# Performance work log

Hardware: AMD Instinct MI355X
Metric: run time of the kernel (lower is better)

Reference implementation:

```python
import jax, jax.numpy as jnp
import numpy as np

LATENT_DIM = 128
KQ_DIM = 32
B, N, K = 4, 16384, 64


def setup_inputs() -> dict:
    key = jax.random.key(0)
    k1, k2, k3, k4, k5, k6, k7 = jax.random.split(key, 7)
    return {
        "indices": jax.random.randint(k1, (3, B, N, K), 0, N, dtype=jnp.int64)
        if jax.config.jax_enable_x64 else jax.random.randint(k1, (3, B, N, K), 0, N, dtype=jnp.int32),
        "img": jax.random.normal(k2, (B, 3, 128, 128), dtype=jnp.float32),
        "features": jax.random.normal(k3, (B, N, LATENT_DIM), dtype=jnp.float32),
        "Wk": jax.random.normal(k4, (KQ_DIM, LATENT_DIM), dtype=jnp.float32) * 0.05,
        "bk": jax.random.normal(k5, (KQ_DIM,), dtype=jnp.float32) * 0.05,
        "Wq": jax.random.normal(k6, (KQ_DIM, LATENT_DIM), dtype=jnp.float32) * 0.05,
        "bq": jax.random.normal(k7, (KQ_DIM,), dtype=jnp.float32) * 0.05,
    }


def reference(indices, img, features, Wk, bk, Wq, bq):
    # features: [B, N, latent] -> keys/queries: [B, N, D]
    ks = jnp.einsum("bnl,dl->bnd", features, Wk) + bk
    qs = jnp.einsum("bnl,dl->bnd", features, Wq) + bq
    D = ks.shape[-1]
    # indices row 1 indexes keys, row 2 indexes queries (values in [0, N))
    x_idx = indices[1].reshape(B, N * K)  # [B, N*K]
    y_idx = indices[2].reshape(B, N * K)
    # gather along node axis: [B, N*K, D]
    x_feat = jnp.take_along_axis(ks, x_idx[:, :, None], axis=1)
    y_feat = jnp.take_along_axis(qs, y_idx[:, :, None], axis=1)
    # scaled dot product per edge -> [B, N, K]
    logits = (x_feat * y_feat).sum(axis=-1).reshape(B, N, K) * (D ** -0.5)
    return logits
```

## Files before the change

kernel.cpp:

```cpp
#include <hip/hip_runtime.h>
#include <hip/hip_fp16.h>

#define LATENT 128
#define DQK    32
#define BB     4
#define NN     16384
#define KK     64
#define TOTAL_EDGES (BB * NN * KK)
#define TOTAL_NODES (BB * NN)
#define PADF   132
#define EPT    4

__device__ __forceinline__ int dot4i8(int a, int b, int c) {
#if __has_builtin(__builtin_amdgcn_sdot4)
    return __builtin_amdgcn_sdot4(a, b, c, false);
#else
    c += ((a << 24) >> 24) * ((b << 24) >> 24);
    c += ((a << 16) >> 24) * ((b << 16) >> 24);
    c += ((a <<  8) >> 24) * ((b <<  8) >> 24);
    c += (a >> 24) * (b >> 24);
    return c;
#endif
}

__global__ __launch_bounds__(256, 2) void proj_kernel(
    const float* __restrict__ features,
    const float* __restrict__ Wk,
    const float* __restrict__ bk,
    const float* __restrict__ Wq,
    const float* __restrict__ bq,
    signed char* __restrict__ ks8,
    signed char* __restrict__ qs8,
    __half* __restrict__ sk,
    __half* __restrict__ sq)
{
    __shared__ float sf[64 * PADF];
    __shared__ float sw[64 * PADF];
    __shared__ float sb[64];

    const int t = threadIdx.x;
    const int node0 = blockIdx.x * 64;

    #pragma unroll
    for (int j = 0; j < 8; ++j) {
        int idx = t + j * 256;
        int r = idx >> 5;
        int c = idx & 31;
        const float4* src = (r < 32) ? (const float4*)Wk : (const float4*)Wq;
        float4 v = src[(size_t)(r & 31) * 32 + c];
        *(float4*)&sw[r * PADF + c * 4] = v;
    }
    if (t < 64) sb[t] = (t < 32) ? bk[t] : bq[t - 32];

    #pragma unroll
    for (int j = 0; j < 8; ++j) {
        int idx = t + j * 256;
        int r = idx >> 5;
        int c = idx & 31;
        float4 v = ((const float4*)(features + (size_t)(node0 + r) * LATENT))[c];
        *(float4*)&sf[r * PADF + c * 4] = v;
    }
    __syncthreads();

    const int tx = t & 15;
    const int ty = t >> 4;

    float acc[4][4];
    #pragma unroll
    for (int i = 0; i < 4; ++i)
        #pragma unroll
        for (int u = 0; u < 4; ++u) acc[i][u] = 0.f;

    #pragma unroll 4
    for (int kk = 0; kk < 32; ++kk) {
        float4 a[4], b[4];
        #pragma unroll
        for (int i = 0; i < 4; ++i)
            a[i] = *(const float4*)&sf[(ty * 4 + i) * PADF + kk * 4];
        #pragma unroll
        for (int u = 0; u < 4; ++u)
            b[u] = *(const float4*)&sw[(tx + 16 * u) * PADF + kk * 4];
        #pragma unroll
        for (int i = 0; i < 4; ++i)
            #pragma unroll
            for (int u = 0; u < 4; ++u)
                acc[i][u] += a[i].x * b[u].x + a[i].y * b[u].y
                           + a[i].z * b[u].z + a[i].w * b[u].w;
    }

    float vk0[4], vk1[4], vq0[4], vq1[4], mk[4], mq[4];
    #pragma unroll
    for (int i = 0; i < 4; ++i) {
        vk0[i] = acc[i][0] + sb[tx];
        vk1[i] = acc[i][1] + sb[tx + 16];
        vq0[i] = acc[i][2] + sb[tx + 32];
        vq1[i] = acc[i][3] + sb[tx + 48];
        mk[i] = fmaxf(fabsf(vk0[i]), fabsf(vk1[i]));
        mq[i] = fmaxf(fabsf(vq0[i]), fabsf(vq1[i]));
    }
    #pragma unroll
    for (int mask = 1; mask < 16; mask <<= 1) {
        #pragma unroll
        for (int i = 0; i < 4; ++i) {
            mk[i] = fmaxf(mk[i], __shfl_xor(mk[i], mask));
            mq[i] = fmaxf(mq[i], __shfl_xor(mq[i], mask));
        }
    }
    #pragma unroll
    for (int i = 0; i < 4; ++i) {
        const int node = node0 + ty * 4 + i;
        const float invk = (mk[i] > 0.f) ? 127.f / mk[i] : 0.f;
        const float invq = (mq[i] > 0.f) ? 127.f / mq[i] : 0.f;
        signed char* kr = ks8 + (size_t)node * 32;
        signed char* qr = qs8 + (size_t)node * 32;
        kr[tx]      = (signed char)__float2int_rn(vk0[i] * invk);
        kr[tx + 16] = (signed char)__float2int_rn(vk1[i] * invk);
        qr[tx]      = (signed char)__float2int_rn(vq0[i] * invq);
        qr[tx + 16] = (signed char)__float2int_rn(vq1[i] * invq);
        if (tx == 0) {
            sk[node] = __float2half(mk[i] * (1.f / 127.f));
            sq[node] = __float2half(mq[i] * (1.f / 127.f));
        }
    }
}

__global__ __launch_bounds__(512, 2) void edge_kernel(
    const int* __restrict__ xidx,
    const int* __restrict__ yidx,
    const signed char* __restrict__ ks8,
    const signed char* __restrict__ qs8,
    const __half* __restrict__ sk,
    const __half* __restrict__ sq,
    float* __restrict__ out)
{
    __shared__ __half ssk[NN];
    __shared__ __half ssq[NN];

    const int t = threadIdx.x;
    const int b = blockIdx.x >> 9;

    const uint4* gk = (const uint4*)(sk + (size_t)b * NN);
    const uint4* gq = (const uint4*)(sq + (size_t)b * NN);
    uint4* lk = (uint4*)ssk;
    uint4* lq = (uint4*)ssq;
    #pragma unroll
    for (int j = 0; j < 4; ++j) {
        lk[t + j * 512] = gk[t + j * 512];
        lq[t + j * 512] = gq[t + j * 512];
    }
    __syncthreads();

    const int base_e = (blockIdx.x & 511) * (512 * EPT);
    const int gbase  = b << 20;
    const size_t nodebase = (size_t)b << 14;

    int xs[EPT], ys[EPT];
    #pragma unroll
    for (int m = 0; m < EPT; ++m) {
        const int e = base_e + m * 512 + t;
        xs[m] = xidx[gbase + e];
        ys[m] = yidx[gbase + e];
    }
    __builtin_amdgcn_sched_barrier(0);

    uint4 kv0[EPT], kv1[EPT], qv0[EPT], qv1[EPT];
    const uint4* k4 = (const uint4*)ks8;
    const uint4* q4 = (const uint4*)qs8;
    #pragma unroll
    for (int m = 0; m < EPT; ++m) {
        const size_t xo = (nodebase + (size_t)xs[m]) << 1;
        const size_t yo = (nodebase + (size_t)ys[m]) << 1;
        kv0[m] = k4[xo];
        kv1[m] = k4[xo + 1];
        qv0[m] = q4[yo];
        qv1[m] = q4[yo + 1];
    }
    __builtin_amdgcn_sched_barrier(0);

    #pragma unroll
    for (int m = 0; m < EPT; ++m) {
        int d = 0;
        d = dot4i8((int)kv0[m].x, (int)qv0[m].x, d);
        d = dot4i8((int)kv0[m].y, (int)qv0[m].y, d);
        d = dot4i8((int)kv0[m].z, (int)qv0[m].z, d);
        d = dot4i8((int)kv0[m].w, (int)qv0[m].w, d);
        d = dot4i8((int)kv1[m].x, (int)qv1[m].x, d);
        d = dot4i8((int)kv1[m].y, (int)qv1[m].y, d);
        d = dot4i8((int)kv1[m].z, (int)qv1[m].z, d);
        d = dot4i8((int)kv1[m].w, (int)qv1[m].w, d);
        const float skx = __half2float(ssk[xs[m]]);
        const float sqy = __half2float(ssq[ys[m]]);
        const int e = base_e + m * 512 + t;
        out[gbase + e] = (float)d * skx * sqy * 0.17677669529663687f;
    }
}

extern "C" void kernel_launch(void* const* d_in, const int* in_sizes, int n_in,
                              void* d_out, int out_size, void* d_ws, size_t ws_size,
                              hipStream_t stream) {
    const int*   indices  = (const int*)d_in[0];
    const float* features = (const float*)d_in[2];
    const float* Wk       = (const float*)d_in[3];
    const float* bk       = (const float*)d_in[4];
    const float* Wq       = (const float*)d_in[5];
    const float* bq       = (const float*)d_in[6];
    float* out = (float*)d_out;

    signed char* ks8 = (signed char*)d_ws;
    signed char* qs8 = ks8 + (size_t)TOTAL_NODES * 32;
    __half* sk = (__half*)(qs8 + (size_t)TOTAL_NODES * 32);
    __half* sq = sk + TOTAL_NODES;

    const int* xidx = indices + (size_t)1 * TOTAL_EDGES;
    const int* yidx = indices + (size_t)2 * TOTAL_EDGES;

    proj_kernel<<<TOTAL_NODES / 64, 256, 0, stream>>>(
        features, Wk, bk, Wq, bq, ks8, qs8, sk, sq);
    edge_kernel<<<BB * 512, 512, 0, stream>>>(xidx, yidx, ks8, qs8, sk, sq, out);
}
```

Before: 74.24 us.

## Pipeline projection and edge stages per batch in a fused staged kernel

```diff
diff --git a/kernel.cpp b/kernel.cpp
--- a/kernel.cpp
+++ b/kernel.cpp
@@ -10,6 +10,8 @@
 #define TOTAL_NODES (BB * NN)
 #define PADF   132
 #define EPT    4
+#define PROJ_BLOCKS 256
+#define EDGE_BLOCKS 512
 
 __device__ __forceinline__ int dot4i8(int a, int b, int c) {
 #if __has_builtin(__builtin_amdgcn_sdot4)
@@ -23,175 +25,173 @@
 #endif
 }
 
-__global__ __launch_bounds__(256, 2) void proj_kernel(
+__global__ __launch_bounds__(512, 2) void stage_kernel(
     const float* __restrict__ features,
     const float* __restrict__ Wk,
     const float* __restrict__ bk,
     const float* __restrict__ Wq,
     const float* __restrict__ bq,
+    const int* __restrict__ xidx,
+    const int* __restrict__ yidx,
     signed char* __restrict__ ks8,
     signed char* __restrict__ qs8,
     __half* __restrict__ sk,
-    __half* __restrict__ sq)
+    __half* __restrict__ sq,
+    float* __restrict__ out,
+    int eb, int pb, int nProj)
 {
-    __shared__ float sf[64 * PADF];
-    __shared__ float sw[64 * PADF];
-    __shared__ float sb[64];
+    __shared__ __align__(16) unsigned char smem[67840];
 
     const int t = threadIdx.x;
-    const int node0 = blockIdx.x * 64;
-
-    #pragma unroll
-    for (int j = 0; j < 8; ++j) {
-        int idx = t + j * 256;
-        int r = idx >> 5;
-        int c = idx & 31;
-        const float4* src = (r < 32) ? (const float4*)Wk : (const float4*)Wq;
-        float4 v = src[(size_t)(r & 31) * 32 + c];
-        *(float4*)&sw[r * PADF + c * 4] = v;
-    }
-    if (t < 64) sb[t] = (t < 32) ? bk[t] : bq[t - 32];
-
-    #pragma unroll
-    for (int j = 0; j < 8; ++j) {
-        int idx = t + j * 256;
-        int r = idx >> 5;
-        int c = idx & 31;
-        float4 v = ((const float4*)(features + (size_t)(node0 + r) * LATENT))[c];
-        *(float4*)&sf[r * PADF + c * 4] = v;
-    }
-    __syncthreads();
-
-    const int tx = t & 15;
-    const int ty = t >> 4;
-
-    float acc[4][4];
-    #pragma unroll
-    for (int i = 0; i < 4; ++i)
-        #pragma unroll
-        for (int u = 0; u < 4; ++u) acc[i][u] = 0.f;
-
-    #pragma unroll 4
-    for (int kk = 0; kk < 32; ++kk) {
-        float4 a[4], b[4];
-        #pragma unroll
-        for (int i = 0; i < 4; ++i)
-            a[i] = *(const float4*)&sf[(ty * 4 + i) * PADF + kk * 4];
-        #pragma unroll
-        for (int u = 0; u < 4; ++u)
-            b[u] = *(const float4*)&sw[(tx + 16 * u) * PADF + kk * 4];
-        #pragma unroll
-        for (int i = 0; i < 4; ++i)
+
+    if ((int)blockIdx.x < nProj) {
+        float* sf = (float*)smem;
+        float* sw = sf + 64 * PADF;
+        float* sb = sw + 64 * PADF;
+
+        const int node0 = (pb << 14) + blockIdx.x * 64;
+
+        #pragma unroll
+        for (int j = 0; j < 4; ++j) {
+            int idx = t + j * 512;
+            int r = idx >> 5;
+            int c = idx & 31;
+            const float4* src = (r < 32) ? (const float4*)Wk : (const float4*)Wq;
+            float4 v = src[(size_t)(r & 31) * 32 + c];
+            *(float4*)&sw[r * PADF + c * 4] = v;
+        }
+        if (t < 64) sb[t] = (t < 32) ? bk[t] : bq[t - 32];
+
+        #pragma unroll
+        for (int j = 0; j < 4; ++j) {
+            int idx = t + j * 512;
+            int r = idx >> 5;
+            int c = idx & 31;
+            float4 v = ((const float4*)(features + (size_t)(node0 + r) * LATENT))[c];
+            *(float4*)&sf[r * PADF + c * 4] = v;
+        }
+        __syncthreads();
+
+        const int tx = t & 15;
+        const int ty = t >> 4;
+
+        float acc[2][4];
+        #pragma unroll
+        for (int i = 0; i < 2; ++i)
+            #pragma unroll
+            for (int u = 0; u < 4; ++u) acc[i][u] = 0.f;
+
+        #pragma unroll 4
+        for (int kk = 0; kk < 32; ++kk) {
+            float4 a[2], b[4];
+            #pragma unroll
+            for (int i = 0; i < 2; ++i)
+                a[i] = *(const float4*)&sf[(ty * 2 + i) * PADF + kk * 4];
             #pragma unroll
             for (int u = 0; u < 4; ++u)
-                acc[i][u] += a[i].x * b[u].x + a[i].y * b[u].y
-                           + a[i].z * b[u].z + a[i].w * b[u].w;
-    }
-
-    float vk0[4], vk1[4], vq0[4], vq1[4], mk[4], mq[4];
-    #pragma unroll
-    for (int i = 0; i < 4; ++i) {
-        vk0[i] = acc[i][0] + sb[tx];
-        vk1[i] = acc[i][1] + sb[tx + 16];
-        vq0[i] = acc[i][2] + sb[tx + 32];
-        vq1[i] = acc[i][3] + sb[tx + 48];
-        mk[i] = fmaxf(fabsf(vk0[i]), fabsf(vk1[i]));
-        mq[i] = fmaxf(fabsf(vq0[i]), fabsf(vq1[i]));
-    }
-    #pragma unroll
-    for (int mask = 1; mask < 16; mask <<= 1) {
-        #pragma unroll
-        for (int i = 0; i < 4; ++i) {
-            mk[i] = fmaxf(mk[i], __shfl_xor(mk[i], mask));
-            mq[i] = fmaxf(mq[i], __shfl_xor(mq[i], mask));
-        }
-    }
-    #pragma unroll
-    for (int i = 0; i < 4; ++i) {
-        const int node = node0 + ty * 4 + i;
-        const float invk = (mk[i] > 0.f) ? 127.f / mk[i] : 0.f;
-        const float invq = (mq[i] > 0.f) ? 127.f / mq[i] : 0.f;
-        signed char* kr = ks8 + (size_t)node * 32;
-        signed char* qr = qs8 + (size_t)node * 32;
-        kr[tx]      = (signed char)__float2int_rn(vk0[i] * invk);
-        kr[tx + 16] = (signed char)__float2int_rn(vk1[i] * invk);
-        qr[tx]      = (signed char)__float2int_rn(vq0[i] * invq);
-        qr[tx + 16] = (signed char)__float2int_rn(vq1[i] * invq);
-        if (tx == 0) {
-            sk[node] = __float2half(mk[i] * (1.f / 127.f));
-            sq[node] = __float2half(mq[i] * (1.f / 127.f));
-        }
-    }
-}
-
-__global__ __launch_bounds__(512, 2) void edge_kernel(
-    const int* __restrict__ xidx,
-    const int* __restrict__ yidx,
-    const signed char* __restrict__ ks8,
-    const signed char* __restrict__ qs8,
-    const __half* __restrict__ sk,
-    const __half* __restrict__ sq,
-    float* __restrict__ out)
-{
-    __shared__ __half ssk[NN];
-    __shared__ __half ssq[NN];
-
-    const int t = threadIdx.x;
-    const int b = blockIdx.x >> 9;
-
-    const uint4* gk = (const uint4*)(sk + (size_t)b * NN);
-    const uint4* gq = (const uint4*)(sq + (size_t)b * NN);
-    uint4* lk = (uint4*)ssk;
-    uint4* lq = (uint4*)ssq;
-    #pragma unroll
-    for (int j = 0; j < 4; ++j) {
-        lk[t + j * 512] = gk[t + j * 512];
-        lq[t + j * 512] = gq[t + j * 512];
-    }
-    __syncthreads();
-
-    const int base_e = (blockIdx.x & 511) * (512 * EPT);
-    const int gbase  = b << 20;
-    const size_t nodebase = (size_t)b << 14;
-
-    int xs[EPT], ys[EPT];
-    #pragma unroll
-    for (int m = 0; m < EPT; ++m) {
-        const int e = base_e + m * 512 + t;
-        xs[m] = xidx[gbase + e];
-        ys[m] = yidx[gbase + e];
-    }
-    __builtin_amdgcn_sched_barrier(0);
-
-    uint4 kv0[EPT], kv1[EPT], qv0[EPT], qv1[EPT];
-    const uint4* k4 = (const uint4*)ks8;
-    const uint4* q4 = (const uint4*)qs8;
-    #pragma unroll
-    for (int m = 0; m < EPT; ++m) {
-        const size_t xo = (nodebase + (size_t)xs[m]) << 1;
-        const size_t yo = (nodebase + (size_t)ys[m]) << 1;
-        kv0[m] = k4[xo];
-        kv1[m] = k4[xo + 1];
-        qv0[m] = q4[yo];
-        qv1[m] = q4[yo + 1];
-    }
-    __builtin_amdgcn_sched_barrier(0);
-
-    #pragma unroll
-    for (int m = 0; m < EPT; ++m) {
-        int d = 0;
-        d = dot4i8((int)kv0[m].x, (int)qv0[m].x, d);
-        d = dot4i8((int)kv0[m].y, (int)qv0[m].y, d);
-        d = dot4i8((int)kv0[m].z, (int)qv0[m].z, d);
-        d = dot4i8((int)kv0[m].w, (int)qv0[m].w, d);
-        d = dot4i8((int)kv1[m].x, (int)qv1[m].x, d);
-        d = dot4i8((int)kv1[m].y, (int)qv1[m].y, d);
-        d = dot4i8((int)kv1[m].z, (int)qv1[m].z, d);
-        d = dot4i8((int)kv1[m].w, (int)qv1[m].w, d);
-        const float skx = __half2float(ssk[xs[m]]);
-        const float sqy = __half2float(ssq[ys[m]]);
-        const int e = base_e + m * 512 + t;
-        out[gbase + e] = (float)d * skx * sqy * 0.17677669529663687f;
+                b[u] = *(const float4*)&sw[(tx + 16 * u) * PADF + kk * 4];
+            #pragma unroll
+            for (int i = 0; i < 2; ++i)
+                #pragma unroll
+                for (int u = 0; u < 4; ++u)
+                    acc[i][u] += a[i].x * b[u].x + a[i].y * b[u].y
+                               + a[i].z * b[u].z + a[i].w * b[u].w;
+        }
+
+        float vk0[2], vk1[2], vq0[2], vq1[2], mk[2], mq[2];
+        #pragma unroll
+        for (int i = 0; i < 2; ++i) {
+            vk0[i] = acc[i][0] + sb[tx];
+            vk1[i] = acc[i][1] + sb[tx + 16];
+            vq0[i] = acc[i][2] + sb[tx + 32];
+            vq1[i] = acc[i][3] + sb[tx + 48];
+            mk[i] = fmaxf(fabsf(vk0[i]), fabsf(vk1[i]));
+            mq[i] = fmaxf(fabsf(vq0[i]), fabsf(vq1[i]));
+        }
+        #pragma unroll
+        for (int mask = 1; mask < 16; mask <<= 1) {
+            #pragma unroll
+            for (int i = 0; i < 2; ++i) {
+                mk[i] = fmaxf(mk[i], __shfl_xor(mk[i], mask));
+                mq[i] = fmaxf(mq[i], __shfl_xor(mq[i], mask));
+            }
+        }
+        #pragma unroll
+        for (int i = 0; i < 2; ++i) {
+            const int node = node0 + ty * 2 + i;
+            const float invk = (mk[i] > 0.f) ? 127.f / mk[i] : 0.f;
+            const float invq = (mq[i] > 0.f) ? 127.f / mq[i] : 0.f;
+            signed char* kr = ks8 + (size_t)node * 32;
+            signed char* qr = qs8 + (size_t)node * 32;
+            kr[tx]      = (signed char)__float2int_rn(vk0[i] * invk);
+            kr[tx + 16] = (signed char)__float2int_rn(vk1[i] * invk);
+            qr[tx]      = (signed char)__float2int_rn(vq0[i] * invq);
+            qr[tx + 16] = (signed char)__float2int_rn(vq1[i] * invq);
+            if (tx == 0) {
+                sk[node] = __float2half(mk[i] * (1.f / 127.f));
+                sq[node] = __float2half(mq[i] * (1.f / 127.f));
+            }
+        }
+    } else {
+        __half* ssk = (__half*)smem;
+        __half* ssq = ssk + NN;
+
+        const int ebid = blockIdx.x - nProj;
+
+        const uint4* gk = (const uint4*)(sk + (size_t)eb * NN);
+        const uint4* gq = (const uint4*)(sq + (size_t)eb * NN);
+        uint4* lk = (uint4*)ssk;
+        uint4* lq = (uint4*)ssq;
+        #pragma unroll
+        for (int j = 0; j < 4; ++j) {
+            lk[t + j * 512] = gk[t + j * 512];
+            lq[t + j * 512] = gq[t + j * 512];
+        }
+        __syncthreads();
+
+        const int base_e = ebid * (512 * EPT);
+        const int gbase  = eb << 20;
+        const size_t nodebase = (size_t)eb << 14;
+
+        int xs[EPT], ys[EPT];
+        #pragma unroll
+        for (int m = 0; m < EPT; ++m) {
+            const int e = base_e + m * 512 + t;
+            xs[m] = xidx[gbase + e];
+            ys[m] = yidx[gbase + e];
+        }
+        __builtin_amdgcn_sched_barrier(0);
+
+        uint4 kv0[EPT], kv1[EPT], qv0[EPT], qv1[EPT];
+        const uint4* k4 = (const uint4*)ks8;
+        const uint4* q4 = (const uint4*)qs8;
+        #pragma unroll
+        for (int m = 0; m < EPT; ++m) {
+            const size_t xo = (nodebase + (size_t)xs[m]) << 1;
+            const size_t yo = (nodebase + (size_t)ys[m]) << 1;
+            kv0[m] = k4[xo];
+            kv1[m] = k4[xo + 1];
+            qv0[m] = q4[yo];
+            qv1[m] = q4[yo + 1];
+        }
+        __builtin_amdgcn_sched_barrier(0);
+
+        #pragma unroll
+        for (int m = 0; m < EPT; ++m) {
+            int d = 0;
+            d = dot4i8((int)kv0[m].x, (int)qv0[m].x, d);
+            d = dot4i8((int)kv0[m].y, (int)qv0[m].y, d);
+            d = dot4i8((int)kv0[m].z, (int)qv0[m].z, d);
+            d = dot4i8((int)kv0[m].w, (int)qv0[m].w, d);
+            d = dot4i8((int)kv1[m].x, (int)qv1[m].x, d);
+            d = dot4i8((int)kv1[m].y, (int)qv1[m].y, d);
+            d = dot4i8((int)kv1[m].z, (int)qv1[m].z, d);
+            d = dot4i8((int)kv1[m].w, (int)qv1[m].w, d);
+            const float skx = __half2float(ssk[xs[m]]);
+            const float sqy = __half2float(ssq[ys[m]]);
+            const int e = base_e + m * 512 + t;
+            out[gbase + e] = (float)d * skx * sqy * 0.17677669529663687f;
+        }
     }
 }
 
@@ -214,7 +214,13 @@
     const int* xidx = indices + (size_t)1 * TOTAL_EDGES;
     const int* yidx = indices + (size_t)2 * TOTAL_EDGES;
 
-    proj_kernel<<<TOTAL_NODES / 64, 256, 0, stream>>>(
-        features, Wk, bk, Wq, bq, ks8, qs8, sk, sq);
-    edge_kernel<<<BB * 512, 512, 0, stream>>>(xidx, yidx, ks8, qs8, sk, sq, out);
+    for (int s = 0; s < 5; ++s) {
+        const int eb = s - 1;
+        const int pb = s;
+        const int nProj = (pb < BB) ? PROJ_BLOCKS : 0;
+        const int nEdge = (eb >= 0) ? EDGE_BLOCKS : 0;
+        stage_kernel<<<nProj + nEdge, 512, 0, stream>>>(
+            features, Wk, bk, Wq, bq, xidx, yidx, ks8, qs8, sk, sq, out,
+            eb, pb, nProj);
+    }
 }
```

New measurement: 83.96 us. +13.1%, slower.

## Fuse projection and edge kernels into one cooperative kernel with grid sync

Applied to the files above, without the earlier changes.

```diff
diff --git a/kernel.cpp b/kernel.cpp
--- a/kernel.cpp
+++ b/kernel.cpp
@@ -1,5 +1,8 @@
 #include <hip/hip_runtime.h>
 #include <hip/hip_fp16.h>
+#include <hip/hip_cooperative_groups.h>
+
+namespace cg = cooperative_groups;
 
 #define LATENT 128
 #define DQK    32
@@ -9,7 +12,9 @@
 #define TOTAL_EDGES (BB * NN * KK)
 #define TOTAL_NODES (BB * NN)
 #define PADF   132
+#define PADH   132
 #define EPT    4
+#define COOP_BLOCKS 256
 
 __device__ __forceinline__ int dot4i8(int a, int b, int c) {
 #if __has_builtin(__builtin_amdgcn_sdot4)
@@ -23,15 +28,199 @@
 #endif
 }
 
-__global__ __launch_bounds__(256, 2) void proj_kernel(
+__global__ __launch_bounds__(512, 2) void fused_kernel(
     const float* __restrict__ features,
     const float* __restrict__ Wk,
     const float* __restrict__ bk,
     const float* __restrict__ Wq,
     const float* __restrict__ bq,
+    const int* __restrict__ xidx,
+    const int* __restrict__ yidx,
     signed char* __restrict__ ks8,
     signed char* __restrict__ qs8,
     __half* __restrict__ sk,
+    __half* __restrict__ sq,
+    float* __restrict__ out)
+{
+    __shared__ __align__(16) unsigned char smem[65536];
+
+    const int t = threadIdx.x;
+    const int bid = blockIdx.x;
+
+    {
+        float*  sf  = (float*)smem;
+        __half* swh = (__half*)(sf + 64 * PADF);
+        float*  sb  = (float*)(swh + 64 * PADH);
+
+        #pragma unroll
+        for (int j = 0; j < 4; ++j) {
+            int idx = t + j * 512;
+            int r = idx >> 5;
+            int c = idx & 31;
+            const float4* src = (r < 32) ? (const float4*)Wk : (const float4*)Wq;
+            float4 v = src[(size_t)(r & 31) * 32 + c];
+            *(__half2*)&swh[r * PADH + c * 4]     = __floats2half2_rn(v.x, v.y);
+            *(__half2*)&swh[r * PADH + c * 4 + 2] = __floats2half2_rn(v.z, v.w);
+        }
+        if (t < 64) sb[t] = (t < 32) ? bk[t] : bq[t - 32];
+
+        const int tx = t & 15;
+        const int ty = t >> 4;
+
+        for (int tile = 0; tile < 4; ++tile) {
+            const int node0 = bid * 256 + tile * 64;
+
+            __syncthreads();
+            #pragma unroll
+            for (int j = 0; j < 4; ++j) {
+                int idx = t + j * 512;
+                int r = idx >> 5;
+                int c = idx & 31;
+                float4 v = ((const float4*)(features + (size_t)(node0 + r) * LATENT))[c];
+                *(float4*)&sf[r * PADF + c * 4] = v;
+            }
+            __syncthreads();
+
+            float acc[2][4];
+            #pragma unroll
+            for (int i = 0; i < 2; ++i)
+                #pragma unroll
+                for (int u = 0; u < 4; ++u) acc[i][u] = 0.f;
+
+            #pragma unroll 4
+            for (int kk = 0; kk < 32; ++kk) {
+                float4 a[2], b[4];
+                #pragma unroll
+                for (int i = 0; i < 2; ++i)
+                    a[i] = *(const float4*)&sf[(ty * 2 + i) * PADF + kk * 4];
+                #pragma unroll
+                for (int u = 0; u < 4; ++u) {
+                    const int row = tx + 16 * u;
+                    float2 f01 = __half22float2(*(const __half2*)&swh[row * PADH + kk * 4]);
+                    float2 f23 = __half22float2(*(const __half2*)&swh[row * PADH + kk * 4 + 2]);
+                    b[u] = make_float4(f01.x, f01.y, f23.x, f23.y);
+                }
+                #pragma unroll
+                for (int i = 0; i < 2; ++i)
+                    #pragma unroll
+                    for (int u = 0; u < 4; ++u)
+                        acc[i][u] += a[i].x * b[u].x + a[i].y * b[u].y
+                                   + a[i].z * b[u].z + a[i].w * b[u].w;
+            }
+
+            float vk0[2], vk1[2], vq0[2], vq1[2], mk[2], mq[2];
+            #pragma unroll
+            for (int i = 0; i < 2; ++i) {
+                vk0[i] = acc[i][0] + sb[tx];
+                vk1[i] = acc[i][1] + sb[tx + 16];
+                vq0[i] = acc[i][2] + sb[tx + 32];
+                vq1[i] = acc[i][3] + sb[tx + 48];
+                mk[i] = fmaxf(fabsf(vk0[i]), fabsf(vk1[i]));
+                mq[i] = fmaxf(fabsf(vq0[i]), fabsf(vq1[i]));
+            }
+            #pragma unroll
+            for (int mask = 1; mask < 16; mask <<= 1) {
+                #pragma unroll
+                for (int i = 0; i < 2; ++i) {
+                    mk[i] = fmaxf(mk[i], __shfl_xor(mk[i], mask));
+                    mq[i] = fmaxf(mq[i], __shfl_xor(mq[i], mask));
+                }
+            }
+            #pragma unroll
+            for (int i = 0; i < 2; ++i) {
+                const int node = node0 + ty * 2 + i;
+                const float invk = (mk[i] > 0.f) ? 127.f / mk[i] : 0.f;
+                const float invq = (mq[i] > 0.f) ? 127.f / mq[i] : 0.f;
+                signed char* kr = ks8 + (size_t)node * 32;
+                signed char* qr = qs8 + (size_t)node * 32;
+                kr[tx]      = (signed char)__float2int_rn(vk0[i] * invk);
+                kr[tx + 16] = (signed char)__float2int_rn(vk1[i] * invk);
+                qr[tx]      = (signed char)__float2int_rn(vq0[i] * invq);
+                qr[tx + 16] = (signed char)__float2int_rn(vq1[i] * invq);
+                if (tx == 0) {
+                    sk[node] = __float2half(mk[i] * (1.f / 127.f));
+                    sq[node] = __float2half(mq[i] * (1.f / 127.f));
+                }
+            }
+        }
+    }
+
+    __threadfence();
+    cg::this_grid().sync();
+
+    {
+        __half* ssk = (__half*)smem;
+        __half* ssq = ssk + NN;
+
+        const int b = bid >> 6;
+        const int lbid = bid & 63;
+
+        __syncthreads();
+        const uint4* gk = (const uint4*)(sk + (size_t)b * NN);
+        const uint4* gq = (const uint4*)(sq + (size_t)b * NN);
+        uint4* lk = (uint4*)ssk;
+        uint4* lq = (uint4*)ssq;
+        #pragma unroll
+        for (int j = 0; j < 4; ++j) {
+            lk[t + j * 512] = gk[t + j * 512];
+            lq[t + j * 512] = gq[t + j * 512];
+        }
+        __syncthreads();
+
+        const int gbase = b << 20;
+        const size_t nodebase = (size_t)b << 14;
+        const uint4* k4 = (const uint4*)ks8;
+        const uint4* q4 = (const uint4*)qs8;
+
+        for (int it = 0; it < 8; ++it) {
+            const int base_e = lbid * 16384 + it * 2048;
+
+            int xs[EPT], ys[EPT];
+            #pragma unroll
+            for (int m = 0; m < EPT; ++m) {
+                const int e = base_e + m * 512 + t;
+                xs[m] = xidx[gbase + e];
+                ys[m] = yidx[gbase + e];
+            }
+            __builtin_amdgcn_sched_barrier(0);
+
+            uint4 kv0[EPT], kv1[EPT], qv0[EPT], qv1[EPT];
+            #pragma unroll
+            for (int m = 0; m < EPT; ++m) {
+                const size_t xo = (nodebase + (size_t)xs[m]) << 1;
+                const size_t yo = (nodebase + (size_t)ys[m]) << 1;
+                kv0[m] = k4[xo];
+                kv1[m] = k4[xo + 1];
+                qv0[m] = q4[yo];
+                qv1[m] = q4[yo + 1];
+            }
+            __builtin_amdgcn_sched_barrier(0);
+
+            #pragma unroll
+            for (int m = 0; m < EPT; ++m) {
+                int d = 0;
+                d = dot4i8((int)kv0[m].x, (int)qv0[m].x, d);
+                d = dot4i8((int)kv0[m].y, (int)qv0[m].y, d);
+                d = dot4i8((int)kv0[m].z, (int)qv0[m].z, d);
+                d = dot4i8((int)kv0[m].w, (int)qv0[m].w, d);
+                d = dot4i8((int)kv1[m].x, (int)qv1[m].x, d);
+                d = dot4i8((int)kv1[m].y, (int)qv1[m].y, d);
+                d = dot4i8((int)kv1[m].z, (int)qv1[m].z, d);
+                d = dot4i8((int)kv1[m].w, (int)qv1[m].w, d);
+                const float skx = __half2float(ssk[xs[m]]);
+                const float sqy = __half2float(ssq[ys[m]]);
+                const int e = base_e + m * 512 + t;
+                out[gbase + e] = (float)d * skx * sqy * 0.17677669529663687f;
+            }
+        }
+    }
+}
+
+__global__ __launch_bounds__(256, 2) void proj_kernel(
+    const float* __restrict__ features, const float* __restrict__ Wk,
+    const float* __restrict__ bk, const float* __restrict__ Wq,
+    const float* __restrict__ bq, signed char* __restrict__ ks8,
+    signed char* __restrict__ qs8, __half* __restrict__ sk,
     __half* __restrict__ sq)
 {
     __shared__ float sf[64 * PADF];
@@ -125,12 +314,9 @@
 }
 
 __global__ __launch_bounds__(512, 2) void edge_kernel(
-    const int* __restrict__ xidx,
-    const int* __restrict__ yidx,
-    const signed char* __restrict__ ks8,
-    const signed char* __restrict__ qs8,
-    const __half* __restrict__ sk,
-    const __half* __restrict__ sq,
+    const int* __restrict__ xidx, const int* __restrict__ yidx,
+    const signed char* __restrict__ ks8, const signed char* __restrict__ qs8,
+    const __half* __restrict__ sk, const __half* __restrict__ sq,
     float* __restrict__ out)
 {
     __shared__ __half ssk[NN];
@@ -214,7 +400,17 @@
     const int* xidx = indices + (size_t)1 * TOTAL_EDGES;
     const int* yidx = indices + (size_t)2 * TOTAL_EDGES;
 
-    proj_kernel<<<TOTAL_NODES / 64, 256, 0, stream>>>(
-        features, Wk, bk, Wq, bq, ks8, qs8, sk, sq);
-    edge_kernel<<<BB * 512, 512, 0, stream>>>(xidx, yidx, ks8, qs8, sk, sq, out);
+    void* args[] = {
+        (void*)&features, (void*)&Wk, (void*)&bk, (void*)&Wq, (void*)&bq,
+        (void*)&xidx, (void*)&yidx, (void*)&ks8, (void*)&qs8,
+        (void*)&sk, (void*)&sq, (void*)&out
+    };
+    hipError_t err = hipLaunchCooperativeKernel((const void*)fused_kernel,
+                                                dim3(COOP_BLOCKS), dim3(512),
+                                                args, 0, stream);
+    if (err != hipSuccess) {
+        proj_kernel<<<TOTAL_NODES / 64, 256, 0, stream>>>(
+            features, Wk, bk, Wq, bq, ks8, qs8, sk, sq);
+        edge_kernel<<<BB * 512, 512, 0, stream>>>(xidx, yidx, ks8, qs8, sk, sq, out);
+    }
 }
```

New measurement: 194.0 us. +161.4%, slower.
